# Kernel tuning notes

Hardware: AMD Instinct MI355X
Metric: run time of the kernel (lower is better)

The kernel has to match this reference:

```python
import jax, jax.numpy as jnp
import numpy as np
from jax import lax

_A = -0.75  # PyTorch bicubic coefficient


def _cubic_kernel(x):
    x = np.abs(x)
    return np.where(x <= 1.0, (_A + 2) * x**3 - (_A + 3) * x**2 + 1,
                    np.where(x < 2.0, _A * x**3 - 5 * _A * x**2 + 8 * _A * x - 4 * _A, 0.0))


def _cubic_mat(out_s, in_s):
    # align_corners=True bicubic interpolation matrix [out_s, in_s]
    i = np.arange(out_s)
    s = i * (in_s - 1) / (out_s - 1) if out_s > 1 else np.zeros(out_s)
    f = np.floor(s).astype(np.int64)
    t = s - f
    M = np.zeros((out_s, in_s), dtype=np.float32)
    for off in range(-1, 3):
        idx = np.clip(f + off, 0, in_s - 1)
        np.add.at(M, (i, idx), _cubic_kernel(t - off).astype(np.float32))
    return jnp.asarray(M)


def _bicubic_up(x, out_hw):
    Mh = _cubic_mat(out_hw[0], x.shape[-2])
    Mw = _cubic_mat(out_hw[1], x.shape[-1])
    y = jnp.einsum('Hh,bchw->bcHw', Mh, x)
    return jnp.einsum('Ww,bcHw->bcHW', Mw, y)


def _conv(x, w, b, pad=1):
    y = lax.conv_general_dilated(x, w, (1, 1), [(pad, pad), (pad, pad)],
                                 dimension_numbers=('NCHW', 'OIHW', 'NCHW'))
    return y + b[None, :, None, None]


def _pool(x):
    return lax.reduce_window(x, -jnp.inf, lax.max, (1, 1, 2, 2), (1, 1, 2, 2), 'VALID')


def _features(x, ws):
    # VGG19 feat1 = conv0+relu (64ch, full res); feat2 = conv2..conv14 (256ch, 1/4 res)
    x1 = jax.nn.relu(_conv(x, *ws[0]))
    h = jax.nn.relu(_conv(x1, *ws[1]))
    h = _pool(h)
    h = jax.nn.relu(_conv(h, *ws[2]))
    h = jax.nn.relu(_conv(h, *ws[3]))
    h = _pool(h)
    h = jax.nn.relu(_conv(h, *ws[4]))
    h = jax.nn.relu(_conv(h, *ws[5]))
    h = jax.nn.relu(_conv(h, *ws[6]))
    h = _bicubic_up(h, x1.shape[-2:])  # bicubic, align_corners=True
    return jnp.concatenate([x1, h], axis=1)  # 64 + 256 = 320 channels


def _forward(x_ref, x_template, w0, b0, w2, b2, w5, b5, w7, b7, w10, b10, w12, b12,
             w14, b14, coef_ref, coef_temp, fw1, fb1, fw2, fb2, fw3, fb3):
    ws = [(w0, b0), (w2, b2), (w5, b5), (w7, b7), (w10, b10), (w12, b12), (w14, b14)]
    fref = _features(x_ref, ws)
    ftem = _features(x_template, ws)
    # L2-normalize over channel dim
    fref = fref / (1e-8 + jnp.linalg.norm(fref, axis=1, keepdims=True))
    ftem = ftem / (1e-8 + jnp.linalg.norm(ftem, axis=1, keepdims=True))
    b, c, H, W = fref.shape
    fref = fref.reshape(b, c, H // 2, 2, W // 2, 2).mean(axis=(3, 5))
    # dense correlation volume
    dist = jnp.einsum('bcmn,bcpq->bmnpq', fref, ftem) / 320.0
    m, n, p, q = dist.shape[1:]
    dist = dist.reshape(b, m * n, p * q)
    # dual-axis softmax + sqrt combination (LoFTR-style)
    conf_ref = jax.nn.softmax(coef_ref * dist, axis=-2)
    conf_tmp = jax.nn.softmax(coef_temp * dist, axis=-1)
    confidence = jnp.sqrt(conf_ref * conf_tmp)
    conf_values, _ = lax.top_k(confidence, 5)  # [b, m*n, 5]
    conf = conf_values.reshape(b, m, n, 5).transpose(0, 3, 1, 2)
    # final head (dropout = identity in eval)
    h = jax.nn.relu(_conv(conf, fw1, fb1))
    h = jax.nn.relu(_conv(h, fw2, fb2))
    out = _conv(h, fw3, fb3, pad=0)
    out = _bicubic_up(out, x_ref.shape[-2:])
    return out


def setup_inputs() -> dict:
    key = jax.random.key(0)
    ks = jax.random.split(key, 16)
    B, H, W = 1, 128, 128

    def cw(k, o, i, s):
        return jax.random.normal(k, (o, i, s, s), jnp.float32) * (1.0 / np.sqrt(i * s * s))

    d = {
        'x_ref': jax.random.normal(ks[0], (B, 3, H, W), jnp.float32),
        'x_template': jax.random.normal(ks[1], (B, 3, H, W), jnp.float32),
        'w0': cw(ks[2], 64, 3, 3), 'b0': jnp.zeros((64,), jnp.float32),
        'w2': cw(ks[3], 64, 64, 3), 'b2': jnp.zeros((64,), jnp.float32),
        'w5': cw(ks[4], 128, 64, 3), 'b5': jnp.zeros((128,), jnp.float32),
        'w7': cw(ks[5], 128, 128, 3), 'b7': jnp.zeros((128,), jnp.float32),
        'w10': cw(ks[6], 256, 128, 3), 'b10': jnp.zeros((256,), jnp.float32),
        'w12': cw(ks[7], 256, 256, 3), 'b12': jnp.zeros((256,), jnp.float32),
        'w14': cw(ks[8], 256, 256, 3), 'b14': jnp.zeros((256,), jnp.float32),
        'coef_ref': jnp.float32(1.0), 'coef_temp': jnp.float32(1.0),
        # final head: weights_init_normal -> N(1/3, 0.02)
        'fw1': 1.0 / 3 + 0.02 * jax.random.normal(ks[9], (8, 5, 3, 3), jnp.float32),
        'fb1': 0.02 * jax.random.normal(ks[10], (8,), jnp.float32),
        'fw2': 1.0 / 3 + 0.02 * jax.random.normal(ks[11], (8, 8, 3, 3), jnp.float32),
        'fb2': 0.02 * jax.random.normal(ks[12], (8,), jnp.float32),
        'fw3': 1.0 / 3 + 0.02 * jax.random.normal(ks[13], (1, 8, 1, 1), jnp.float32),
        'fb3': 0.02 * jax.random.normal(ks[14], (1,), jnp.float32),
    }
    return d


def reference(x_ref, x_template, w0, b0, w2, b2, w5, b5, w7, b7, w10, b10, w12, b12,
              w14, b14, coef_ref, coef_temp, fw1, fb1, fw2, fb2, fw3, fb3):
    return _forward(x_ref, x_template, w0, b0, w2, b2, w5, b5, w7, b7, w10, b10,
                    w12, b12, w14, b14, coef_ref, coef_temp, fw1, fb1, fw2, fb2, fw3, fb3)
```

## Files before the change

kernel.cpp:

```cpp
#include <hip/hip_runtime.h>
#include <math.h>

typedef unsigned short ushort_t;
typedef unsigned int uint_t;
typedef __attribute__((ext_vector_type(8))) short bf16x8;
typedef __attribute__((ext_vector_type(4))) float f32x4;

#define FSTRIDE ((size_t)16384 * 320)
#define TSTRIDE ((size_t)16384 * 64)

__device__ inline ushort_t f2bf(float f) {
    union { float f; uint_t u; } x; x.f = f;
    uint_t r = x.u + 0x7fffu + ((x.u >> 16) & 1u);
    return (ushort_t)(r >> 16);
}
__device__ inline float bf2f(ushort_t h) {
    union { uint_t u; float f; } x; x.u = ((uint_t)h) << 16;
    return x.f;
}
__device__ inline float bflo(uint_t u) {
    union { uint_t u; float f; } x; x.u = u << 16; return x.f;
}
__device__ inline float bfhi(uint_t u) {
    union { uint_t u; float f; } x; x.u = u & 0xffff0000u; return x.f;
}
__device__ inline uint_t cvtpk_bf16(float lo, float hi) {
    uint_t r;
    asm volatile("v_cvt_pk_bf16_f32 %0, %1, %2" : "=v"(r) : "v"(lo), "v"(hi));
    return r;
}
__device__ inline void gload16(const void* g, void* l) {
    __builtin_amdgcn_global_load_lds(
        (const __attribute__((address_space(1))) void*)g,
        (__attribute__((address_space(3))) void*)l, 16, 0, 0);
}

__global__ void wtrans_k(const float* __restrict__ w, ushort_t* __restrict__ wT, int CO, int CI)
{
    int idx = blockIdx.x * 256 + threadIdx.x;
    if (idx >= CO * CI * 9) return;
    int tap = idx % 9;
    int rem = idx / 9;
    int ci = rem % CI;
    int co = rem / CI;
    wT[((size_t)tap * CO + co) * CI + ci] = f2bf(w[idx]);
}

__global__ __launch_bounds__(256) void conv0_k(const float* __restrict__ x0, const float* __restrict__ x1,
                                               const float* __restrict__ w,
                                               const float* __restrict__ b, ushort_t* __restrict__ F)
{
    const float* x = blockIdx.y ? x1 : x0;
    F += (size_t)blockIdx.y * FSTRIDE;
    int co = threadIdx.x & 63;
    int p = blockIdx.x * 4 + (threadIdx.x >> 6);
    int y = p >> 7, xx = p & 127;
    float acc = b[co];
#pragma unroll
    for (int ci = 0; ci < 3; ++ci) {
#pragma unroll
        for (int t = 0; t < 9; ++t) {
            int dy = t / 3 - 1, dx = t % 3 - 1;
            int yy = y + dy, xc = xx + dx;
            if ((unsigned)yy < 128u && (unsigned)xc < 128u) {
                acc += x[ci * 16384 + yy * 128 + xc] * w[co * 27 + ci * 9 + t];
            }
        }
    }
    F[(size_t)p * 320 + co] = f2bf(fmaxf(acc, 0.f));
}

template<int CI>
__global__ __launch_bounds__(256) void conv_mfma_k(
    const ushort_t* __restrict__ in, int ldin, int inoff, size_t inImgStride,
    const ushort_t* __restrict__ wT, const float* __restrict__ bias,
    ushort_t* __restrict__ out, int ldout, int outoff, size_t outImgStride,
    int H, int W, int CO)
{
    in += (size_t)blockIdx.z * inImgStride;
    out += (size_t)blockIdx.z * outImgStride;
    const int tid = threadIdx.x;
    const int lane = tid & 63, wid = tid >> 6;
    const int wr = wid >> 1, wc = wid & 1;
    const int m0 = blockIdx.x * 64;
    const int n0 = blockIdx.y * 64;
    const int fr = lane & 15;
    const int fo = (lane >> 4) << 3;

    size_t abase[2];
    unsigned vmask[2];
#pragma unroll
    for (int mi = 0; mi < 2; ++mi) {
        int p = m0 + wr * 32 + mi * 16 + fr;
        int y = p / W, x = p % W;
        abase[mi] = (size_t)p * ldin + inoff + fo;
        unsigned vm = 0;
#pragma unroll
        for (int t = 0; t < 9; ++t) {
            int dy = t / 3 - 1, dx = t % 3 - 1;
            if ((unsigned)(y + dy) < (unsigned)H && (unsigned)(x + dx) < (unsigned)W) vm |= 1u << t;
        }
        vmask[mi] = vm;
    }

    f32x4 zero = {0.f, 0.f, 0.f, 0.f};
    f32x4 acc[2][2] = {{zero, zero}, {zero, zero}};
    const bf16x8 zz = {0, 0, 0, 0, 0, 0, 0, 0};

    for (int t = 0; t < 9; ++t) {
        int toff = ((t / 3 - 1) * W + (t % 3 - 1)) * ldin;
        bool v0 = (vmask[0] >> t) & 1u;
        bool v1 = (vmask[1] >> t) & 1u;
        const ushort_t* wp0 = wT + ((size_t)(t * CO + n0 + wc * 32 + fr)) * CI + fo;
        const ushort_t* wp1 = wp0 + (size_t)16 * CI;
#pragma unroll
        for (int kc = 0; kc < CI / 32; ++kc) {
            int k0 = kc * 32;
            bf16x8 a0 = v0 ? *(const bf16x8*)(in + abase[0] + toff + k0) : zz;
            bf16x8 a1 = v1 ? *(const bf16x8*)(in + abase[1] + toff + k0) : zz;
            bf16x8 b0 = *(const bf16x8*)(wp0 + k0);
            bf16x8 b1 = *(const bf16x8*)(wp1 + k0);
            acc[0][0] = __builtin_amdgcn_mfma_f32_16x16x32_bf16(b0, a0, acc[0][0], 0, 0, 0);
            acc[0][1] = __builtin_amdgcn_mfma_f32_16x16x32_bf16(b1, a0, acc[0][1], 0, 0, 0);
            acc[1][0] = __builtin_amdgcn_mfma_f32_16x16x32_bf16(b0, a1, acc[1][0], 0, 0, 0);
            acc[1][1] = __builtin_amdgcn_mfma_f32_16x16x32_bf16(b1, a1, acc[1][1], 0, 0, 0);
        }
    }

#pragma unroll
    for (int mi = 0; mi < 2; ++mi) {
#pragma unroll
        for (int ni = 0; ni < 2; ++ni) {
            int pix = m0 + wr * 32 + mi * 16 + (lane & 15);
            int ch = n0 + wc * 32 + ni * 16 + ((lane >> 4) << 2);
            float4 bv = *(const float4*)(bias + ch);
            float r0 = fmaxf(acc[mi][ni][0] + bv.x, 0.f);
            float r1 = fmaxf(acc[mi][ni][1] + bv.y, 0.f);
            float r2 = fmaxf(acc[mi][ni][2] + bv.z, 0.f);
            float r3 = fmaxf(acc[mi][ni][3] + bv.w, 0.f);
            uint2 pk;
            pk.x = (uint_t)f2bf(r0) | ((uint_t)f2bf(r1) << 16);
            pk.y = (uint_t)f2bf(r2) | ((uint_t)f2bf(r3) << 16);
            *(uint2*)(out + (size_t)pix * ldout + outoff + ch) = pk;
        }
    }
}

template<int CI>
__global__ __launch_bounds__(64) void conv_mfma1w_k(
    const ushort_t* __restrict__ in, int ldin, size_t inImgStride,
    const ushort_t* __restrict__ wT, const float* __restrict__ bias,
    ushort_t* __restrict__ out, int ldout, size_t outImgStride,
    int H, int W, int CO)
{
    in += (size_t)blockIdx.z * inImgStride;
    out += (size_t)blockIdx.z * outImgStride;
    const int lane = threadIdx.x;
    const int m0 = blockIdx.x * 32;
    const int n0 = blockIdx.y * 32;
    const int fr = lane & 15;
    const int fo = (lane >> 4) << 3;

    size_t abase[2];
    unsigned vmask[2];
#pragma unroll
    for (int mi = 0; mi < 2; ++mi) {
        int p = m0 + mi * 16 + fr;
        int y = p / W, x = p % W;
        abase[mi] = (size_t)p * ldin + fo;
        unsigned vm = 0;
#pragma unroll
        for (int t = 0; t < 9; ++t) {
            int dy = t / 3 - 1, dx = t % 3 - 1;
            if ((unsigned)(y + dy) < (unsigned)H && (unsigned)(x + dx) < (unsigned)W) vm |= 1u << t;
        }
        vmask[mi] = vm;
    }

    f32x4 zero = {0.f, 0.f, 0.f, 0.f};
    f32x4 acc[2][2] = {{zero, zero}, {zero, zero}};
    const bf16x8 zz = {0, 0, 0, 0, 0, 0, 0, 0};

    for (int t = 0; t < 9; ++t) {
        int toff = ((t / 3 - 1) * W + (t % 3 - 1)) * ldin;
        bool v0 = (vmask[0] >> t) & 1u;
        bool v1 = (vmask[1] >> t) & 1u;
        const ushort_t* wp0 = wT + ((size_t)(t * CO + n0 + fr)) * CI + fo;
        const ushort_t* wp1 = wp0 + (size_t)16 * CI;
#pragma unroll
        for (int kc = 0; kc < CI / 32; ++kc) {
            int k0 = kc * 32;
            bf16x8 a0 = v0 ? *(const bf16x8*)(in + abase[0] + toff + k0) : zz;
            bf16x8 a1 = v1 ? *(const bf16x8*)(in + abase[1] + toff + k0) : zz;
            bf16x8 b0 = *(const bf16x8*)(wp0 + k0);
            bf16x8 b1 = *(const bf16x8*)(wp1 + k0);
            acc[0][0] = __builtin_amdgcn_mfma_f32_16x16x32_bf16(b0, a0, acc[0][0], 0, 0, 0);
            acc[0][1] = __builtin_amdgcn_mfma_f32_16x16x32_bf16(b1, a0, acc[0][1], 0, 0, 0);
            acc[1][0] = __builtin_amdgcn_mfma_f32_16x16x32_bf16(b0, a1, acc[1][0], 0, 0, 0);
            acc[1][1] = __builtin_amdgcn_mfma_f32_16x16x32_bf16(b1, a1, acc[1][1], 0, 0, 0);
        }
    }

#pragma unroll
    for (int mi = 0; mi < 2; ++mi) {
#pragma unroll
        for (int ni = 0; ni < 2; ++ni) {
            int pix = m0 + mi * 16 + (lane & 15);
            int ch = n0 + ni * 16 + ((lane >> 4) << 2);
            float4 bv = *(const float4*)(bias + ch);
            float r0 = fmaxf(acc[mi][ni][0] + bv.x, 0.f);
            float r1 = fmaxf(acc[mi][ni][1] + bv.y, 0.f);
            float r2 = fmaxf(acc[mi][ni][2] + bv.z, 0.f);
            float r3 = fmaxf(acc[mi][ni][3] + bv.w, 0.f);
            uint2 pk;
            pk.x = (uint_t)f2bf(r0) | ((uint_t)f2bf(r1) << 16);
            pk.y = (uint_t)f2bf(r2) | ((uint_t)f2bf(r3) << 16);
            *(uint2*)(out + (size_t)pix * ldout + ch) = pk;
        }
    }
}

__global__ void maxpool_nhwc_k(const ushort_t* __restrict__ in, ushort_t* __restrict__ out,
                               int C, int Hi, int Wi)
{
    in += (size_t)blockIdx.y * TSTRIDE;
    out += (size_t)blockIdx.y * TSTRIDE;
    int idx = blockIdx.x * 256 + threadIdx.x;
    int CG = C >> 3;
    int Wo = Wi >> 1, Ho = Hi >> 1;
    if (idx >= Ho * Wo * CG) return;
    int cg = idx % CG;
    int p = idx / CG;
    int y = p / Wo, x = p % Wo;
    const ushort_t* ip = in + ((size_t)(2 * y) * Wi + 2 * x) * C + cg * 8;
    bf16x8 v0 = *(const bf16x8*)(ip);
    bf16x8 v1 = *(const bf16x8*)(ip + C);
    bf16x8 v2 = *(const bf16x8*)(ip + (size_t)Wi * C);
    bf16x8 v3 = *(const bf16x8*)(ip + (size_t)Wi * C + C);
    bf16x8 r;
#pragma unroll
    for (int j = 0; j < 8; ++j) {
        float m = fmaxf(fmaxf(bf2f((ushort_t)v0[j]), bf2f((ushort_t)v1[j])),
                        fmaxf(bf2f((ushort_t)v2[j]), bf2f((ushort_t)v3[j])));
        r[j] = (short)f2bf(m);
    }
    *(bf16x8*)(out + (size_t)p * C + cg * 8) = r;
}

__device__ inline void cubw(float t, float* w) {
    float x0 = 1.f + t, x2 = 1.f - t, x3 = 2.f - t;
    w[0] = ((-0.75f*x0 + 3.75f)*x0 - 6.f)*x0 + 3.f;
    w[1] = (1.25f*t - 2.25f)*t*t + 1.f;
    w[2] = (1.25f*x2 - 2.25f)*x2*x2 + 1.f;
    w[3] = ((-0.75f*x3 + 3.75f)*x3 - 6.f)*x3 + 3.f;
}

__global__ __launch_bounds__(256) void bicubic_nhwc_k(const ushort_t* __restrict__ in, ushort_t* __restrict__ F)
{
    in += (size_t)blockIdx.y * TSTRIDE;
    F += (size_t)blockIdx.y * FSTRIDE;
    int idx = blockIdx.x * 256 + threadIdx.x;
    int cg = idx & 31;
    int p = idx >> 5;
    int Y = p >> 7, X = p & 127;
    float sy = (float)Y * (31.f / 127.f);
    float sx = (float)X * (31.f / 127.f);
    int fy = (int)floorf(sy), fx = (int)floorf(sx);
    float ty = sy - (float)fy, tx = sx - (float)fx;
    float wy[4], wx[4];
    cubw(ty, wy); cubw(tx, wx);
    float a[8] = {0.f, 0.f, 0.f, 0.f, 0.f, 0.f, 0.f, 0.f};
#pragma unroll
    for (int i = 0; i < 4; ++i) {
        int yy = min(max(fy - 1 + i, 0), 31);
#pragma unroll
        for (int j = 0; j < 4; ++j) {
            int xx = min(max(fx - 1 + j, 0), 31);
            float w = wy[i] * wx[j];
            bf16x8 v = *(const bf16x8*)(in + ((size_t)yy * 32 + xx) * 256 + cg * 8);
#pragma unroll
            for (int e = 0; e < 8; ++e) a[e] += w * bf2f((ushort_t)v[e]);
        }
    }
    bf16x8 r;
#pragma unroll
    for (int e = 0; e < 8; ++e) r[e] = (short)f2bf(a[e]);
    *(bf16x8*)(F + (size_t)p * 320 + 64 + cg * 8) = r;
}

__global__ __launch_bounds__(256) void norm_k(ushort_t* __restrict__ F)
{
    int lane = threadIdx.x & 63;
    int p = blockIdx.x * 4 + (threadIdx.x >> 6);
    ushort_t* rp = F + (size_t)p * 320;
    bool act = lane < 40;
    bf16x8 v = {0, 0, 0, 0, 0, 0, 0, 0};
    float ss = 0.f;
    if (act) {
        v = *(const bf16x8*)(rp + lane * 8);
#pragma unroll
        for (int e = 0; e < 8; ++e) { float f = bf2f((ushort_t)v[e]); ss += f * f; }
    }
#pragma unroll
    for (int off = 32; off > 0; off >>= 1) ss += __shfl_xor(ss, off);
    float inv = 1.f / (1e-8f + sqrtf(ss));
    if (act) {
#pragma unroll
        for (int e = 0; e < 8; ++e) v[e] = (short)f2bf(bf2f((ushort_t)v[e]) * inv);
        *(bf16x8*)(rp + lane * 8) = v;
    }
}

__global__ void pool_ref_nhwc_k(const ushort_t* __restrict__ F, ushort_t* __restrict__ A)
{
    int idx = blockIdx.x * 256 + threadIdx.x;
    if (idx >= 4096 * 40) return;
    int cg = idx % 40;
    int m = idx / 40;
    int y = m >> 6, x = m & 63;
    const ushort_t* ip = F + ((size_t)(2 * y) * 128 + 2 * x) * 320 + cg * 8;
    bf16x8 v0 = *(const bf16x8*)(ip);
    bf16x8 v1 = *(const bf16x8*)(ip + 320);
    bf16x8 v2 = *(const bf16x8*)(ip + 128 * 320);
    bf16x8 v3 = *(const bf16x8*)(ip + 128 * 320 + 320);
    bf16x8 r;
#pragma unroll
    for (int j = 0; j < 8; ++j) {
        float s = bf2f((ushort_t)v0[j]) + bf2f((ushort_t)v1[j]) + bf2f((ushort_t)v2[j]) + bf2f((ushort_t)v3[j]);
        r[j] = (short)f2bf(0.25f * s);
    }
    *(bf16x8*)(A + (size_t)m * 320 + cg * 8) = r;
}

__global__ __launch_bounds__(256) void gemm_corr_k(
    const ushort_t* __restrict__ A, const ushort_t* __restrict__ B, ushort_t* __restrict__ D,
    const float* __restrict__ coefr, const float* __restrict__ coeft,
    float* __restrict__ rpsum, float* __restrict__ cpsum)
{
    __shared__ ushort_t lA[3][128 * 32];
    __shared__ ushort_t lB[3][128 * 32];
    __shared__ float cl[2][128];
    __shared__ float rl[2][128];
    const int tid = threadIdx.x;
    const int lane = tid & 63;
    const int wid = tid >> 6;
    const int wr = wid >> 1, wc = wid & 1;
    const int m0 = blockIdx.y * 128, n0 = blockIdx.x * 128;
    const int fr = lane & 15;
    const int fo = (lane >> 4) << 3;
    const int srow = tid >> 2;
    const int scol = (tid & 3) << 3;

    const ushort_t* Ag0 = A + (size_t)(m0 + srow) * 320 + scol;
    const ushort_t* Ag1 = Ag0 + (size_t)64 * 320;
    const ushort_t* Bg0 = B + (size_t)(n0 + srow) * 320 + scol;
    const ushort_t* Bg1 = Bg0 + (size_t)64 * 320;

    f32x4 zero = {0.f, 0.f, 0.f, 0.f};
    f32x4 acc[4][4];
#pragma unroll
    for (int i = 0; i < 4; ++i)
#pragma unroll
        for (int j = 0; j < 4; ++j) acc[i][j] = zero;

#define STAGE(buf, kk) { \
        gload16(Ag0 + (kk), &lA[buf][wid * 512]); \
        gload16(Ag1 + (kk), &lA[buf][2048 + wid * 512]); \
        gload16(Bg0 + (kk), &lB[buf][wid * 512]); \
        gload16(Bg1 + (kk), &lB[buf][2048 + wid * 512]); }

#define COMPUTE(buf) { \
        bf16x8 af[4], bfr[4]; \
        _Pragma("unroll") \
        for (int mi = 0; mi < 4; ++mi) \
            af[mi] = *(const bf16x8*)&lA[buf][(wr * 64 + mi * 16 + fr) * 32 + fo]; \
        _Pragma("unroll") \
        for (int ni = 0; ni < 4; ++ni) \
            bfr[ni] = *(const bf16x8*)&lB[buf][(wc * 64 + ni * 16 + fr) * 32 + fo]; \
        _Pragma("unroll") \
        for (int mi = 0; mi < 4; ++mi) \
            _Pragma("unroll") \
            for (int ni = 0; ni < 4; ++ni) \
                acc[mi][ni] = __builtin_amdgcn_mfma_f32_16x16x32_bf16(bfr[ni], af[mi], acc[mi][ni], 0, 0, 0); }

    STAGE(0, 0)
    STAGE(1, 32)
#pragma unroll
    for (int t = 0; t < 10; ++t) {
        if (t < 9) {
            asm volatile("s_waitcnt vmcnt(4)" ::: "memory");
        } else {
            asm volatile("s_waitcnt vmcnt(0)" ::: "memory");
        }
        __builtin_amdgcn_s_barrier();
        if (t + 2 < 10) {
            STAGE((t + 2) % 3, 32 * (t + 2))
        }
        COMPUTE(t % 3)
    }
#undef STAGE
#undef COMPUTE

    const float s = 1.0f / 320.0f;
    const float cr = coefr[0], ct = coeft[0];
    const bool sameCoef = (cr == ct);
    float rpx[4] = {0.f, 0.f, 0.f, 0.f};
    float cpx[4][4];
#pragma unroll
    for (int ni = 0; ni < 4; ++ni)
#pragma unroll
        for (int r = 0; r < 4; ++r) cpx[ni][r] = 0.f;

    const int mrow = lane & 15;
    const int ng = (lane >> 4) << 2;
#pragma unroll
    for (int mi = 0; mi < 4; ++mi) {
        int m = m0 + wr * 64 + mi * 16 + mrow;
        ushort_t* drow = D + (size_t)m * 16384;
#pragma unroll
        for (int ni = 0; ni < 4; ++ni) {
            int n = n0 + wc * 64 + ni * 16 + ng;
            float d0 = acc[mi][ni][0] * s;
            float d1 = acc[mi][ni][1] * s;
            float d2 = acc[mi][ni][2] * s;
            float d3 = acc[mi][ni][3] * s;
            uint2 pk;
            pk.x = cvtpk_bf16(d0, d1);
            pk.y = cvtpk_bf16(d2, d3);
            *(uint2*)(drow + n) = pk;
            float e0 = __expf(cr * d0), e1 = __expf(cr * d1);
            float e2 = __expf(cr * d2), e3 = __expf(cr * d3);
            cpx[ni][0] += e0; cpx[ni][1] += e1; cpx[ni][2] += e2; cpx[ni][3] += e3;
            if (sameCoef) {
                rpx[mi] += e0 + e1 + e2 + e3;
            } else {
                rpx[mi] += __expf(ct * d0) + __expf(ct * d1) + __expf(ct * d2) + __expf(ct * d3);
            }
        }
    }
#pragma unroll
    for (int mi = 0; mi < 4; ++mi) {
        rpx[mi] += __shfl_xor(rpx[mi], 16);
        rpx[mi] += __shfl_xor(rpx[mi], 32);
    }
    if (lane < 16) {
#pragma unroll
        for (int mi = 0; mi < 4; ++mi)
            rl[wc][wr * 64 + mi * 16 + lane] = rpx[mi];
    }
#pragma unroll
    for (int ni = 0; ni < 4; ++ni)
#pragma unroll
        for (int r = 0; r < 4; ++r) {
            cpx[ni][r] += __shfl_xor(cpx[ni][r], 1);
            cpx[ni][r] += __shfl_xor(cpx[ni][r], 2);
            cpx[ni][r] += __shfl_xor(cpx[ni][r], 4);
            cpx[ni][r] += __shfl_xor(cpx[ni][r], 8);
        }
    if ((lane & 15) == 0) {
        int g = lane >> 4;
#pragma unroll
        for (int ni = 0; ni < 4; ++ni)
#pragma unroll
            for (int r = 0; r < 4; ++r)
                cl[wr][wc * 64 + ni * 16 + g * 4 + r] = cpx[ni][r];
    }
    __syncthreads();
    if (tid < 128) {
        cpsum[(size_t)blockIdx.y * 16384 + n0 + tid] = cl[0][tid] + cl[1][tid];
        rpsum[(size_t)blockIdx.x * 4096 + m0 + tid] = rl[0][tid] + rl[1][tid];
    }
}

__global__ void colfin_k(const float* __restrict__ cpsum, float* __restrict__ lc)
{
    int j = blockIdx.x * 256 + threadIdx.x;
    float s = 0.f;
#pragma unroll
    for (int k = 0; k < 32; ++k) s += cpsum[(size_t)k * 16384 + j];
    lc[j] = -0.5f * __logf(s);
}
__global__ void rowfin_k(const float* __restrict__ rpsum, float* __restrict__ invr)
{
    int m = blockIdx.x * 256 + threadIdx.x;
    float s = 0.f;
#pragma unroll
    for (int k = 0; k < 128; ++k) s += rpsum[(size_t)k * 4096 + m];
    invr[m] = rsqrtf(s);
}

#define INS5(w_) { float w = (w_); float mx; \
    mx = fmaxf(w, t0); w = fminf(w, t0); t0 = mx; \
    mx = fmaxf(w, t1); w = fminf(w, t1); t1 = mx; \
    mx = fmaxf(w, t2); w = fminf(w, t2); t2 = mx; \
    mx = fmaxf(w, t3); w = fminf(w, t3); t3 = mx; \
    t4 = fmaxf(w, t4); }

__global__ __launch_bounds__(256) void row_topk_k(
    const ushort_t* __restrict__ Dist, const float* __restrict__ lc,
    const float* __restrict__ invr,
    const float* __restrict__ coefr, const float* __restrict__ coeft,
    float* __restrict__ conf5)
{
    int wid = threadIdx.x >> 6, lane = threadIdx.x & 63;
    int row = blockIdx.x * 4 + wid;
    float hc = 0.5f * (coefr[0] + coeft[0]);
    const ushort_t* rp = Dist + (size_t)row * 16384;

    float t0 = -1e30f, t1 = -1e30f, t2 = -1e30f, t3 = -1e30f, t4 = -1e30f;
    for (int i = 0; i < 32; ++i) {
        int col = (i * 64 + lane) * 8;
        uint4 u = *(const uint4*)(rp + col);
        float4 l0 = *(const float4*)(lc + col);
        float4 l1 = *(const float4*)(lc + col + 4);
        float k0 = fmaf(hc, bflo(u.x), l0.x);
        float k1 = fmaf(hc, bfhi(u.x), l0.y);
        float k2 = fmaf(hc, bflo(u.y), l0.z);
        float k3 = fmaf(hc, bfhi(u.y), l0.w);
        float k4 = fmaf(hc, bflo(u.z), l1.x);
        float k5 = fmaf(hc, bfhi(u.z), l1.y);
        float k6 = fmaf(hc, bflo(u.w), l1.z);
        float k7 = fmaf(hc, bfhi(u.w), l1.w);
        float m8 = fmaxf(fmaxf(fmaxf(k0, k1), fmaxf(k2, k3)),
                         fmaxf(fmaxf(k4, k5), fmaxf(k6, k7)));
        if (m8 > t4) {
            INS5(k0); INS5(k1); INS5(k2); INS5(k3);
            INS5(k4); INS5(k5); INS5(k6); INS5(k7);
        }
    }
#pragma unroll
    for (int off = 1; off < 64; off <<= 1) {
        float o0 = __shfl_xor(t0, off), o1 = __shfl_xor(t1, off), o2 = __shfl_xor(t2, off);
        float o3 = __shfl_xor(t3, off), o4 = __shfl_xor(t4, off);
        INS5(o0); INS5(o1); INS5(o2); INS5(o3); INS5(o4);
    }
    if (lane == 0) {
        float iv = invr[row];
        conf5[0 * 4096 + row] = __expf(t0) * iv;
        conf5[1 * 4096 + row] = __expf(t1) * iv;
        conf5[2 * 4096 + row] = __expf(t2) * iv;
        conf5[3 * 4096 + row] = __expf(t3) * iv;
        conf5[4 * 4096 + row] = __expf(t4) * iv;
    }
}

__global__ void conv3x3_k(const float* __restrict__ in, const float* __restrict__ wgt,
                          const float* __restrict__ bias, float* __restrict__ out,
                          int Cin, int H, int W, int relu)
{
    int p = blockIdx.x * 256 + threadIdx.x;
    int HW = H * W;
    if (p >= HW) return;
    int co0 = blockIdx.y * 8;
    int y = p / W, x = p - y * W;
    float acc0 = bias[co0+0], acc1 = bias[co0+1], acc2 = bias[co0+2], acc3 = bias[co0+3];
    float acc4 = bias[co0+4], acc5 = bias[co0+5], acc6 = bias[co0+6], acc7 = bias[co0+7];
    bool ym = y > 0, yp = y < H-1, xm = x > 0, xp = x < W-1;
    for (int ci = 0; ci < Cin; ++ci) {
        const float* ip = in + (size_t)ci * HW + p;
        float v0 = (ym && xm) ? ip[-W-1] : 0.f;
        float v1 = (ym)       ? ip[-W]   : 0.f;
        float v2 = (ym && xp) ? ip[-W+1] : 0.f;
        float v3 = (xm)       ? ip[-1]   : 0.f;
        float v4 =              ip[0];
        float v5 = (xp)       ? ip[1]    : 0.f;
        float v6 = (yp && xm) ? ip[W-1]  : 0.f;
        float v7 = (yp)       ? ip[W]    : 0.f;
        float v8 = (yp && xp) ? ip[W+1]  : 0.f;
        const float* wp = wgt + ((size_t)co0 * Cin + ci) * 9;
        size_t ws = (size_t)Cin * 9;
#define CACC(q, a) { const float* wq = wp + q * ws; \
        a += wq[0]*v0 + wq[1]*v1 + wq[2]*v2 + wq[3]*v3 + wq[4]*v4 \
           + wq[5]*v5 + wq[6]*v6 + wq[7]*v7 + wq[8]*v8; }
        CACC(0, acc0) CACC(1, acc1) CACC(2, acc2) CACC(3, acc3)
        CACC(4, acc4) CACC(5, acc5) CACC(6, acc6) CACC(7, acc7)
#undef CACC
    }
#define CW(q, a) { float r = a; if (relu) r = fmaxf(r, 0.f); out[(size_t)(co0+q)*HW + p] = r; }
    CW(0, acc0) CW(1, acc1) CW(2, acc2) CW(3, acc3)
    CW(4, acc4) CW(5, acc5) CW(6, acc6) CW(7, acc7)
#undef CW
}

__global__ void bicubic_k(const float* __restrict__ in, float* __restrict__ out,
                          int C, int Hin, int Win, int Hout, int Wout)
{
    int idx = blockIdx.x * 256 + threadIdx.x;
    int total = C * Hout * Wout;
    if (idx >= total) return;
    int X = idx % Wout;
    int Y = (idx / Wout) % Hout;
    int c = idx / (Wout * Hout);
    float sy = (float)Y * (float)(Hin - 1) / (float)(Hout - 1);
    float sx = (float)X * (float)(Win - 1) / (float)(Wout - 1);
    int fy = (int)floorf(sy), fx = (int)floorf(sx);
    float ty = sy - (float)fy, tx = sx - (float)fx;
    float wy[4], wx[4];
    cubw(ty, wy); cubw(tx, wx);
    const float* ip = in + (size_t)c * Hin * Win;
    float acc = 0.f;
#pragma unroll
    for (int i = 0; i < 4; ++i) {
        int yy = min(max(fy - 1 + i, 0), Hin - 1);
        float ra = 0.f;
#pragma unroll
        for (int j = 0; j < 4; ++j) {
            int xx = min(max(fx - 1 + j, 0), Win - 1);
            ra += wx[j] * ip[yy * Win + xx];
        }
        acc += wy[i] * ra;
    }
    out[idx] = acc;
}

__global__ void conv1x1_k(const float* __restrict__ in, const float* __restrict__ w,
                          const float* __restrict__ b, float* __restrict__ out, int Cin, int HW)
{
    int p = blockIdx.x * 256 + threadIdx.x;
    if (p >= HW) return;
    float a = b[0];
    for (int c = 0; c < Cin; ++c) a += w[c] * in[(size_t)c * HW + p];
    out[p] = a;
}

extern "C" void kernel_launch(void* const* d_in, const int* in_sizes, int n_in,
                              void* d_out, int out_size, void* d_ws, size_t ws_size,
                              hipStream_t stream)
{
    const float* x_ref = (const float*)d_in[0];
    const float* x_tem = (const float*)d_in[1];
    const float* w0  = (const float*)d_in[2];   const float* b0  = (const float*)d_in[3];
    const float* w2  = (const float*)d_in[4];   const float* b2  = (const float*)d_in[5];
    const float* w5  = (const float*)d_in[6];   const float* b5  = (const float*)d_in[7];
    const float* w7  = (const float*)d_in[8];   const float* b7  = (const float*)d_in[9];
    const float* w10 = (const float*)d_in[10];  const float* b10 = (const float*)d_in[11];
    const float* w12 = (const float*)d_in[12];  const float* b12 = (const float*)d_in[13];
    const float* w14 = (const float*)d_in[14];  const float* b14 = (const float*)d_in[15];
    const float* coefr = (const float*)d_in[16];
    const float* coeft = (const float*)d_in[17];
    const float* fw1 = (const float*)d_in[18];  const float* fb1 = (const float*)d_in[19];
    const float* fw2 = (const float*)d_in[20];  const float* fb2 = (const float*)d_in[21];
    const float* fw3 = (const float*)d_in[22];  const float* fb3 = (const float*)d_in[23];
    float* out = (float*)d_out;

    char* wsp = (char*)d_ws;
    auto alloc = [&](size_t bytes) { char* p = wsp; wsp += (bytes + 255) & ~(size_t)255; return p; };
    ushort_t* F     = (ushort_t*)alloc(2 * FSTRIDE * 2);
    ushort_t* t1    = (ushort_t*)alloc(2 * TSTRIDE * 2);
    ushort_t* t2    = (ushort_t*)alloc(2 * TSTRIDE * 2);
    ushort_t* wT2   = (ushort_t*)alloc((size_t)64 * 64 * 9 * 2);
    ushort_t* wT5   = (ushort_t*)alloc((size_t)128 * 64 * 9 * 2);
    ushort_t* wT7   = (ushort_t*)alloc((size_t)128 * 128 * 9 * 2);
    ushort_t* wT10  = (ushort_t*)alloc((size_t)256 * 128 * 9 * 2);
    ushort_t* wT12  = (ushort_t*)alloc((size_t)256 * 256 * 9 * 2);
    ushort_t* wT14  = (ushort_t*)alloc((size_t)256 * 256 * 9 * 2);
    ushort_t* Abuf  = (ushort_t*)alloc((size_t)4096 * 320 * 2);
    ushort_t* dist  = (ushort_t*)alloc((size_t)4096 * 16384 * 2);
    float*    rpsum = (float*)alloc((size_t)128 * 4096 * 4);
    float*    cpsum = (float*)alloc((size_t)32 * 16384 * 4);
    float*    lc    = (float*)alloc(16384 * 4);
    float*    invr  = (float*)alloc(4096 * 4);
    float*    conf5 = (float*)alloc(5 * 4096 * 4);
    float*    h1    = (float*)alloc(8 * 4096 * 4);
    float*    h2    = (float*)alloc(8 * 4096 * 4);
    float*    out64 = (float*)alloc(4096 * 4);
    (void)ws_size; (void)n_in; (void)in_sizes; (void)out_size;

    wtrans_k<<<(64*64*9 + 255)/256, 256, 0, stream>>>(w2, wT2, 64, 64);
    wtrans_k<<<(128*64*9 + 255)/256, 256, 0, stream>>>(w5, wT5, 128, 64);
    wtrans_k<<<(128*128*9 + 255)/256, 256, 0, stream>>>(w7, wT7, 128, 128);
    wtrans_k<<<(256*128*9 + 255)/256, 256, 0, stream>>>(w10, wT10, 256, 128);
    wtrans_k<<<(256*256*9 + 255)/256, 256, 0, stream>>>(w12, wT12, 256, 256);
    wtrans_k<<<(256*256*9 + 255)/256, 256, 0, stream>>>(w14, wT14, 256, 256);

    conv0_k<<<dim3(4096, 2), 256, 0, stream>>>(x_ref, x_tem, w0, b0, F);
    conv_mfma_k<64><<<dim3(256, 1, 2), 256, 0, stream>>>(F, 320, 0, FSTRIDE, wT2, b2, t1, 64, 0, TSTRIDE, 128, 128, 64);
    maxpool_nhwc_k<<<dim3(128, 2), 256, 0, stream>>>(t1, t2, 64, 128, 128);
    conv_mfma_k<64><<<dim3(64, 2, 2), 256, 0, stream>>>(t2, 64, 0, TSTRIDE, wT5, b5, t1, 128, 0, TSTRIDE, 64, 64, 128);
    conv_mfma_k<128><<<dim3(64, 2, 2), 256, 0, stream>>>(t1, 128, 0, TSTRIDE, wT7, b7, t2, 128, 0, TSTRIDE, 64, 64, 128);
    maxpool_nhwc_k<<<dim3(64, 2), 256, 0, stream>>>(t2, t1, 128, 64, 64);
    conv_mfma1w_k<128><<<dim3(32, 8, 2), 64, 0, stream>>>(t1, 128, TSTRIDE, wT10, b10, t2, 256, TSTRIDE, 32, 32, 256);
    conv_mfma1w_k<256><<<dim3(32, 8, 2), 64, 0, stream>>>(t2, 256, TSTRIDE, wT12, b12, t1, 256, TSTRIDE, 32, 32, 256);
    conv_mfma1w_k<256><<<dim3(32, 8, 2), 64, 0, stream>>>(t1, 256, TSTRIDE, wT14, b14, t2, 256, TSTRIDE, 32, 32, 256);
    bicubic_nhwc_k<<<dim3(2048, 2), 256, 0, stream>>>(t2, F);
    norm_k<<<8192, 256, 0, stream>>>(F);

    pool_ref_nhwc_k<<<640, 256, 0, stream>>>(F, Abuf);

    gemm_corr_k<<<dim3(128, 32), 256, 0, stream>>>(Abuf, F + FSTRIDE, dist, coefr, coeft, rpsum, cpsum);

    colfin_k<<<64, 256, 0, stream>>>(cpsum, lc);
    rowfin_k<<<16, 256, 0, stream>>>(rpsum, invr);

    row_topk_k<<<1024, 256, 0, stream>>>(dist, lc, invr, coefr, coeft, conf5);

    conv3x3_k<<<dim3(16, 1), 256, 0, stream>>>(conf5, fw1, fb1, h1, 5, 64, 64, 1);
    conv3x3_k<<<dim3(16, 1), 256, 0, stream>>>(h1, fw2, fb2, h2, 8, 64, 64, 1);
    conv1x1_k<<<16, 256, 0, stream>>>(h2, fw3, fb3, out64, 8, 4096);
    bicubic_k<<<64, 256, 0, stream>>>(out64, out, 1, 64, 64, 128, 128);
}
```

Measured before the change: 410.2 us.

## Use smaller one-wave conv tiles, swizzle GEMM LDS, and fuse small launches

Replaces the 4-wave 64x64 conv kernel and the 1-wave 32x32 kernel with one templated single-wave kernel that covers 16 pixels by 16*NF channels. This launches many more blocks, so more of the GPU is busy on the small feature maps. It also XOR-swizzles the LDS layout in the correlation GEMM to cut bank conflicts. Several tiny launches are merged: the six weight transposes, the row and column finalisers, and the second head conv fused with the 1x1 conv. In exchange, the smaller tiles give less data reuse, so each block reloads more weights and activations.

```diff
diff --git a/kernel.cpp b/kernel.cpp
--- a/kernel.cpp
+++ b/kernel.cpp
@@ -35,15 +35,25 @@
         (__attribute__((address_space(3))) void*)l, 16, 0, 0);
 }
 
-__global__ void wtrans_k(const float* __restrict__ w, ushort_t* __restrict__ wT, int CO, int CI)
-{
-    int idx = blockIdx.x * 256 + threadIdx.x;
+struct WT6 {
+    const float* src[6];
+    ushort_t* dst[6];
+    int co[6], ci[6];
+    int off[6];
+};
+__global__ void wtrans6_k(WT6 a)
+{
+    int b = blockIdx.x, seg = 0;
+#pragma unroll
+    for (int s = 1; s < 6; ++s) if (b >= a.off[s]) seg = s;
+    int idx = (b - a.off[seg]) * 256 + threadIdx.x;
+    int CO = a.co[seg], CI = a.ci[seg];
     if (idx >= CO * CI * 9) return;
     int tap = idx % 9;
     int rem = idx / 9;
     int ci = rem % CI;
     int co = rem / CI;
-    wT[((size_t)tap * CO + co) * CI + ci] = f2bf(w[idx]);
+    a.dst[seg][((size_t)tap * CO + co) * CI + ci] = f2bf(a.src[seg][idx]);
 }
 
 __global__ __launch_bounds__(256) void conv0_k(const float* __restrict__ x0, const float* __restrict__ x1,
@@ -70,8 +80,8 @@
     F[(size_t)p * 320 + co] = f2bf(fmaxf(acc, 0.f));
 }
 
-template<int CI>
-__global__ __launch_bounds__(256) void conv_mfma_k(
+template<int CI, int NF>
+__global__ __launch_bounds__(64) void conv1w_k(
     const ushort_t* __restrict__ in, int ldin, int inoff, size_t inImgStride,
     const ushort_t* __restrict__ wT, const float* __restrict__ bias,
     ushort_t* __restrict__ out, int ldout, int outoff, size_t outImgStride,
@@ -79,144 +89,58 @@
 {
     in += (size_t)blockIdx.z * inImgStride;
     out += (size_t)blockIdx.z * outImgStride;
-    const int tid = threadIdx.x;
-    const int lane = tid & 63, wid = tid >> 6;
-    const int wr = wid >> 1, wc = wid & 1;
-    const int m0 = blockIdx.x * 64;
-    const int n0 = blockIdx.y * 64;
+    const int lane = threadIdx.x;
+    const int m0 = blockIdx.x * 16;
+    const int n0 = blockIdx.y * (16 * NF);
     const int fr = lane & 15;
     const int fo = (lane >> 4) << 3;
 
-    size_t abase[2];
-    unsigned vmask[2];
-#pragma unroll
-    for (int mi = 0; mi < 2; ++mi) {
-        int p = m0 + wr * 32 + mi * 16 + fr;
-        int y = p / W, x = p % W;
-        abase[mi] = (size_t)p * ldin + inoff + fo;
-        unsigned vm = 0;
-#pragma unroll
-        for (int t = 0; t < 9; ++t) {
-            int dy = t / 3 - 1, dx = t % 3 - 1;
-            if ((unsigned)(y + dy) < (unsigned)H && (unsigned)(x + dx) < (unsigned)W) vm |= 1u << t;
-        }
-        vmask[mi] = vm;
+    int p = m0 + fr;
+    int y = p / W, x = p % W;
+    size_t abase = (size_t)p * ldin + inoff + fo;
+    unsigned vm = 0;
+#pragma unroll
+    for (int t = 0; t < 9; ++t) {
+        int dy = t / 3 - 1, dx = t % 3 - 1;
+        if ((unsigned)(y + dy) < (unsigned)H && (unsigned)(x + dx) < (unsigned)W) vm |= 1u << t;
     }
 
     f32x4 zero = {0.f, 0.f, 0.f, 0.f};
-    f32x4 acc[2][2] = {{zero, zero}, {zero, zero}};
+    f32x4 acc[NF];
+#pragma unroll
+    for (int i = 0; i < NF; ++i) acc[i] = zero;
     const bf16x8 zz = {0, 0, 0, 0, 0, 0, 0, 0};
 
+#pragma unroll 3
     for (int t = 0; t < 9; ++t) {
         int toff = ((t / 3 - 1) * W + (t % 3 - 1)) * ldin;
-        bool v0 = (vmask[0] >> t) & 1u;
-        bool v1 = (vmask[1] >> t) & 1u;
-        const ushort_t* wp0 = wT + ((size_t)(t * CO + n0 + wc * 32 + fr)) * CI + fo;
-        const ushort_t* wp1 = wp0 + (size_t)16 * CI;
+        bool v = (vm >> t) & 1u;
+        const ushort_t* wp = wT + ((size_t)(t * CO + n0 + fr)) * CI + fo;
 #pragma unroll
         for (int kc = 0; kc < CI / 32; ++kc) {
             int k0 = kc * 32;
-            bf16x8 a0 = v0 ? *(const bf16x8*)(in + abase[0] + toff + k0) : zz;
-            bf16x8 a1 = v1 ? *(const bf16x8*)(in + abase[1] + toff + k0) : zz;
-            bf16x8 b0 = *(const bf16x8*)(wp0 + k0);
-            bf16x8 b1 = *(const bf16x8*)(wp1 + k0);
-            acc[0][0] = __builtin_amdgcn_mfma_f32_16x16x32_bf16(b0, a0, acc[0][0], 0, 0, 0);
-            acc[0][1] = __builtin_amdgcn_mfma_f32_16x16x32_bf16(b1, a0, acc[0][1], 0, 0, 0);
-            acc[1][0] = __builtin_amdgcn_mfma_f32_16x16x32_bf16(b0, a1, acc[1][0], 0, 0, 0);
-            acc[1][1] = __builtin_amdgcn_mfma_f32_16x16x32_bf16(b1, a1, acc[1][1], 0, 0, 0);
-        }
-    }
-
-#pragma unroll
-    for (int mi = 0; mi < 2; ++mi) {
-#pragma unroll
-        for (int ni = 0; ni < 2; ++ni) {
-            int pix = m0 + wr * 32 + mi * 16 + (lane & 15);
-            int ch = n0 + wc * 32 + ni * 16 + ((lane >> 4) << 2);
-            float4 bv = *(const float4*)(bias + ch);
-            float r0 = fmaxf(acc[mi][ni][0] + bv.x, 0.f);
-            float r1 = fmaxf(acc[mi][ni][1] + bv.y, 0.f);
-            float r2 = fmaxf(acc[mi][ni][2] + bv.z, 0.f);
-            float r3 = fmaxf(acc[mi][ni][3] + bv.w, 0.f);
-            uint2 pk;
-            pk.x = (uint_t)f2bf(r0) | ((uint_t)f2bf(r1) << 16);
-            pk.y = (uint_t)f2bf(r2) | ((uint_t)f2bf(r3) << 16);
-            *(uint2*)(out + (size_t)pix * ldout + outoff + ch) = pk;
-        }
-    }
-}
-
-template<int CI>
-__global__ __launch_bounds__(64) void conv_mfma1w_k(
-    const ushort_t* __restrict__ in, int ldin, size_t inImgStride,
-    const ushort_t* __restrict__ wT, const float* __restrict__ bias,
-    ushort_t* __restrict__ out, int ldout, size_t outImgStride,
-    int H, int W, int CO)
-{
-    in += (size_t)blockIdx.z * inImgStride;
-    out += (size_t)blockIdx.z * outImgStride;
-    const int lane = threadIdx.x;
-    const int m0 = blockIdx.x * 32;
-    const int n0 = blockIdx.y * 32;
-    const int fr = lane & 15;
-    const int fo = (lane >> 4) << 3;
-
-    size_t abase[2];
-    unsigned vmask[2];
-#pragma unroll
-    for (int mi = 0; mi < 2; ++mi) {
-        int p = m0 + mi * 16 + fr;
-        int y = p / W, x = p % W;
-        abase[mi] = (size_t)p * ldin + fo;
-        unsigned vm = 0;
-#pragma unroll
-        for (int t = 0; t < 9; ++t) {
-            int dy = t / 3 - 1, dx = t % 3 - 1;
-            if ((unsigned)(y + dy) < (unsigned)H && (unsigned)(x + dx) < (unsigned)W) vm |= 1u << t;
-        }
-        vmask[mi] = vm;
-    }
-
-    f32x4 zero = {0.f, 0.f, 0.f, 0.f};
-    f32x4 acc[2][2] = {{zero, zero}, {zero, zero}};
-    const bf16x8 zz = {0, 0, 0, 0, 0, 0, 0, 0};
-
-    for (int t = 0; t < 9; ++t) {
-        int toff = ((t / 3 - 1) * W + (t % 3 - 1)) * ldin;
-        bool v0 = (vmask[0] >> t) & 1u;
-        bool v1 = (vmask[1] >> t) & 1u;
-        const ushort_t* wp0 = wT + ((size_t)(t * CO + n0 + fr)) * CI + fo;
-        const ushort_t* wp1 = wp0 + (size_t)16 * CI;
-#pragma unroll
-        for (int kc = 0; kc < CI / 32; ++kc) {
-            int k0 = kc * 32;
-            bf16x8 a0 = v0 ? *(const bf16x8*)(in + abase[0] + toff + k0) : zz;
-            bf16x8 a1 = v1 ? *(const bf16x8*)(in + abase[1] + toff + k0) : zz;
-            bf16x8 b0 = *(const bf16x8*)(wp0 + k0);
-            bf16x8 b1 = *(const bf16x8*)(wp1 + k0);
-            acc[0][0] = __builtin_amdgcn_mfma_f32_16x16x32_bf16(b0, a0, acc[0][0], 0, 0, 0);
-            acc[0][1] = __builtin_amdgcn_mfma_f32_16x16x32_bf16(b1, a0, acc[0][1], 0, 0, 0);
-            acc[1][0] = __builtin_amdgcn_mfma_f32_16x16x32_bf16(b0, a1, acc[1][0], 0, 0, 0);
-            acc[1][1] = __builtin_amdgcn_mfma_f32_16x16x32_bf16(b1, a1, acc[1][1], 0, 0, 0);
-        }
-    }
-
-#pragma unroll
-    for (int mi = 0; mi < 2; ++mi) {
-#pragma unroll
-        for (int ni = 0; ni < 2; ++ni) {
-            int pix = m0 + mi * 16 + (lane & 15);
-            int ch = n0 + ni * 16 + ((lane >> 4) << 2);
-            float4 bv = *(const float4*)(bias + ch);
-            float r0 = fmaxf(acc[mi][ni][0] + bv.x, 0.f);
-            float r1 = fmaxf(acc[mi][ni][1] + bv.y, 0.f);
-            float r2 = fmaxf(acc[mi][ni][2] + bv.z, 0.f);
-            float r3 = fmaxf(acc[mi][ni][3] + bv.w, 0.f);
-            uint2 pk;
-            pk.x = (uint_t)f2bf(r0) | ((uint_t)f2bf(r1) << 16);
-            pk.y = (uint_t)f2bf(r2) | ((uint_t)f2bf(r3) << 16);
-            *(uint2*)(out + (size_t)pix * ldout + ch) = pk;
-        }
+            bf16x8 a = v ? *(const bf16x8*)(in + abase + toff + k0) : zz;
+#pragma unroll
+            for (int nf = 0; nf < NF; ++nf) {
+                bf16x8 b = *(const bf16x8*)(wp + (size_t)nf * 16 * CI + k0);
+                acc[nf] = __builtin_amdgcn_mfma_f32_16x16x32_bf16(b, a, acc[nf], 0, 0, 0);
+            }
+        }
+    }
+
+#pragma unroll
+    for (int nf = 0; nf < NF; ++nf) {
+        int pix = m0 + (lane & 15);
+        int ch = n0 + nf * 16 + ((lane >> 4) << 2);
+        float4 bv = *(const float4*)(bias + ch);
+        float r0 = fmaxf(acc[nf][0] + bv.x, 0.f);
+        float r1 = fmaxf(acc[nf][1] + bv.y, 0.f);
+        float r2 = fmaxf(acc[nf][2] + bv.z, 0.f);
+        float r3 = fmaxf(acc[nf][3] + bv.w, 0.f);
+        uint2 pk;
+        pk.x = (uint_t)f2bf(r0) | ((uint_t)f2bf(r1) << 16);
+        pk.y = (uint_t)f2bf(r2) | ((uint_t)f2bf(r3) << 16);
+        *(uint2*)(out + (size_t)pix * ldout + outoff + ch) = pk;
     }
 }
 
@@ -350,10 +274,12 @@
     const int fo = (lane >> 4) << 3;
     const int srow = tid >> 2;
     const int scol = (tid & 3) << 3;
-
-    const ushort_t* Ag0 = A + (size_t)(m0 + srow) * 320 + scol;
+    const int scol_sw = scol ^ ((srow & 3) << 3);
+    const int fo_sw = fo ^ ((fr & 3) << 3);
+
+    const ushort_t* Ag0 = A + (size_t)(m0 + srow) * 320 + scol_sw;
     const ushort_t* Ag1 = Ag0 + (size_t)64 * 320;
-    const ushort_t* Bg0 = B + (size_t)(n0 + srow) * 320 + scol;
+    const ushort_t* Bg0 = B + (size_t)(n0 + srow) * 320 + scol_sw;
     const ushort_t* Bg1 = Bg0 + (size_t)64 * 320;
 
     f32x4 zero = {0.f, 0.f, 0.f, 0.f};
@@ -373,10 +299,10 @@
         bf16x8 af[4], bfr[4]; \
         _Pragma("unroll") \
         for (int mi = 0; mi < 4; ++mi) \
-            af[mi] = *(const bf16x8*)&lA[buf][(wr * 64 + mi * 16 + fr) * 32 + fo]; \
+            af[mi] = *(const bf16x8*)&lA[buf][(wr * 64 + mi * 16 + fr) * 32 + fo_sw]; \
         _Pragma("unroll") \
         for (int ni = 0; ni < 4; ++ni) \
-            bfr[ni] = *(const bf16x8*)&lB[buf][(wc * 64 + ni * 16 + fr) * 32 + fo]; \
+            bfr[ni] = *(const bf16x8*)&lB[buf][(wc * 64 + ni * 16 + fr) * 32 + fo_sw]; \
         _Pragma("unroll") \
         for (int mi = 0; mi < 4; ++mi) \
             _Pragma("unroll") \
@@ -472,21 +398,23 @@
     }
 }
 
-__global__ void colfin_k(const float* __restrict__ cpsum, float* __restrict__ lc)
-{
-    int j = blockIdx.x * 256 + threadIdx.x;
-    float s = 0.f;
-#pragma unroll
-    for (int k = 0; k < 32; ++k) s += cpsum[(size_t)k * 16384 + j];
-    lc[j] = -0.5f * __logf(s);
-}
-__global__ void rowfin_k(const float* __restrict__ rpsum, float* __restrict__ invr)
-{
-    int m = blockIdx.x * 256 + threadIdx.x;
-    float s = 0.f;
-#pragma unroll
-    for (int k = 0; k < 128; ++k) s += rpsum[(size_t)k * 4096 + m];
-    invr[m] = rsqrtf(s);
+__global__ void finboth_k(const float* __restrict__ cpsum, const float* __restrict__ rpsum,
+                          float* __restrict__ lc, float* __restrict__ invr)
+{
+    int b = blockIdx.x;
+    if (b < 64) {
+        int j = b * 256 + threadIdx.x;
+        float s = 0.f;
+#pragma unroll
+        for (int k = 0; k < 32; ++k) s += cpsum[(size_t)k * 16384 + j];
+        lc[j] = -0.5f * __logf(s);
+    } else {
+        int m = (b - 64) * 256 + threadIdx.x;
+        float s = 0.f;
+#pragma unroll
+        for (int k = 0; k < 128; ++k) s += rpsum[(size_t)k * 4096 + m];
+        invr[m] = rsqrtf(s);
+    }
 }
 
 #define INS5(w_) { float w = (w_); float mx; \
@@ -582,6 +510,41 @@
 #undef CW
 }
 
+__global__ void head2_k(const float* __restrict__ in, const float* __restrict__ wgt,
+                        const float* __restrict__ bias, const float* __restrict__ w3,
+                        const float* __restrict__ b3, float* __restrict__ out64)
+{
+    int p = blockIdx.x * 256 + threadIdx.x;
+    int y = p >> 6, x = p & 63;
+    float acc[8];
+#pragma unroll
+    for (int c = 0; c < 8; ++c) acc[c] = bias[c];
+    bool ym = y > 0, yp = y < 63, xm = x > 0, xp = x < 63;
+#pragma unroll
+    for (int ci = 0; ci < 8; ++ci) {
+        const float* ip = in + ci * 4096 + p;
+        float v0 = (ym && xm) ? ip[-65] : 0.f;
+        float v1 = (ym)       ? ip[-64] : 0.f;
+        float v2 = (ym && xp) ? ip[-63] : 0.f;
+        float v3 = (xm)       ? ip[-1]  : 0.f;
+        float v4 =              ip[0];
+        float v5 = (xp)       ? ip[1]   : 0.f;
+        float v6 = (yp && xm) ? ip[63]  : 0.f;
+        float v7 = (yp)       ? ip[64]  : 0.f;
+        float v8 = (yp && xp) ? ip[65]  : 0.f;
+#pragma unroll
+        for (int co = 0; co < 8; ++co) {
+            const float* wq = wgt + ((size_t)co * 8 + ci) * 9;
+            acc[co] += wq[0]*v0 + wq[1]*v1 + wq[2]*v2 + wq[3]*v3 + wq[4]*v4
+                     + wq[5]*v5 + wq[6]*v6 + wq[7]*v7 + wq[8]*v8;
+        }
+    }
+    float o = b3[0];
+#pragma unroll
+    for (int c = 0; c < 8; ++c) o += w3[c] * fmaxf(acc[c], 0.f);
+    out64[p] = o;
+}
+
 __global__ void bicubic_k(const float* __restrict__ in, float* __restrict__ out,
                           int C, int Hin, int Win, int Hout, int Wout)
 {
@@ -611,16 +574,6 @@
         acc += wy[i] * ra;
     }
     out[idx] = acc;
-}
-
-__global__ void conv1x1_k(const float* __restrict__ in, const float* __restrict__ w,
-                          const float* __restrict__ b, float* __restrict__ out, int Cin, int HW)
-{
-    int p = blockIdx.x * 256 + threadIdx.x;
-    if (p >= HW) return;
-    float a = b[0];
-    for (int c = 0; c < Cin; ++c) a += w[c] * in[(size_t)c * HW + p];
-    out[p] = a;
 }
 
 extern "C" void kernel_launch(void* const* d_in, const int* in_sizes, int n_in,
@@ -662,26 +615,29 @@
     float*    invr  = (float*)alloc(4096 * 4);
     float*    conf5 = (float*)alloc(5 * 4096 * 4);
     float*    h1    = (float*)alloc(8 * 4096 * 4);
-    float*    h2    = (float*)alloc(8 * 4096 * 4);
     float*    out64 = (float*)alloc(4096 * 4);
     (void)ws_size; (void)n_in; (void)in_sizes; (void)out_size;
 
-    wtrans_k<<<(64*64*9 + 255)/256, 256, 0, stream>>>(w2, wT2, 64, 64);
-    wtrans_k<<<(128*64*9 + 255)/256, 256, 0, stream>>>(w5, wT5, 128, 64);
-    wtrans_k<<<(128*128*9 + 255)/256, 256, 0, stream>>>(w7, wT7, 128, 128);
-    wtrans_k<<<(256*128*9 + 255)/256, 256, 0, stream>>>(w10, wT10, 256, 128);
-    wtrans_k<<<(256*256*9 + 255)/256, 256, 0, stream>>>(w12, wT12, 256, 256);
-    wtrans_k<<<(256*256*9 + 255)/256, 256, 0, stream>>>(w14, wT14, 256, 256);
+    WT6 wt;
+    wt.src[0] = w2;  wt.dst[0] = wT2;  wt.co[0] = 64;  wt.ci[0] = 64;
+    wt.src[1] = w5;  wt.dst[1] = wT5;  wt.co[1] = 128; wt.ci[1] = 64;
+    wt.src[2] = w7;  wt.dst[2] = wT7;  wt.co[2] = 128; wt.ci[2] = 128;
+    wt.src[3] = w10; wt.dst[3] = wT10; wt.co[3] = 256; wt.ci[3] = 128;
+    wt.src[4] = w12; wt.dst[4] = wT12; wt.co[4] = 256; wt.ci[4] = 256;
+    wt.src[5] = w14; wt.dst[5] = wT14; wt.co[5] = 256; wt.ci[5] = 256;
+    int nblk = 0;
+    for (int s = 0; s < 6; ++s) { wt.off[s] = nblk; nblk += (wt.co[s] * wt.ci[s] * 9 + 255) / 256; }
+    wtrans6_k<<<nblk, 256, 0, stream>>>(wt);
 
     conv0_k<<<dim3(4096, 2), 256, 0, stream>>>(x_ref, x_tem, w0, b0, F);
-    conv_mfma_k<64><<<dim3(256, 1, 2), 256, 0, stream>>>(F, 320, 0, FSTRIDE, wT2, b2, t1, 64, 0, TSTRIDE, 128, 128, 64);
+    conv1w_k<64, 2><<<dim3(1024, 2, 2), 64, 0, stream>>>(F, 320, 0, FSTRIDE, wT2, b2, t1, 64, 0, TSTRIDE, 128, 128, 64);
     maxpool_nhwc_k<<<dim3(128, 2), 256, 0, stream>>>(t1, t2, 64, 128, 128);
-    conv_mfma_k<64><<<dim3(64, 2, 2), 256, 0, stream>>>(t2, 64, 0, TSTRIDE, wT5, b5, t1, 128, 0, TSTRIDE, 64, 64, 128);
-    conv_mfma_k<128><<<dim3(64, 2, 2), 256, 0, stream>>>(t1, 128, 0, TSTRIDE, wT7, b7, t2, 128, 0, TSTRIDE, 64, 64, 128);
+    conv1w_k<64, 2><<<dim3(256, 4, 2), 64, 0, stream>>>(t2, 64, 0, TSTRIDE, wT5, b5, t1, 128, 0, TSTRIDE, 64, 64, 128);
+    conv1w_k<128, 2><<<dim3(256, 4, 2), 64, 0, stream>>>(t1, 128, 0, TSTRIDE, wT7, b7, t2, 128, 0, TSTRIDE, 64, 64, 128);
     maxpool_nhwc_k<<<dim3(64, 2), 256, 0, stream>>>(t2, t1, 128, 64, 64);
-    conv_mfma1w_k<128><<<dim3(32, 8, 2), 64, 0, stream>>>(t1, 128, TSTRIDE, wT10, b10, t2, 256, TSTRIDE, 32, 32, 256);
-    conv_mfma1w_k<256><<<dim3(32, 8, 2), 64, 0, stream>>>(t2, 256, TSTRIDE, wT12, b12, t1, 256, TSTRIDE, 32, 32, 256);
-    conv_mfma1w_k<256><<<dim3(32, 8, 2), 64, 0, stream>>>(t1, 256, TSTRIDE, wT14, b14, t2, 256, TSTRIDE, 32, 32, 256);
+    conv1w_k<128, 1><<<dim3(64, 16, 2), 64, 0, stream>>>(t1, 128, 0, TSTRIDE, wT10, b10, t2, 256, 0, TSTRIDE, 32, 32, 256);
+    conv1w_k<256, 1><<<dim3(64, 16, 2), 64, 0, stream>>>(t2, 256, 0, TSTRIDE, wT12, b12, t1, 256, 0, TSTRIDE, 32, 32, 256);
+    conv1w_k<256, 1><<<dim3(64, 16, 2), 64, 0, stream>>>(t1, 256, 0, TSTRIDE, wT14, b14, t2, 256, 0, TSTRIDE, 32, 32, 256);
     bicubic_nhwc_k<<<dim3(2048, 2), 256, 0, stream>>>(t2, F);
     norm_k<<<8192, 256, 0, stream>>>(F);
 
@@ -689,13 +645,11 @@
 
     gemm_corr_k<<<dim3(128, 32), 256, 0, stream>>>(Abuf, F + FSTRIDE, dist, coefr, coeft, rpsum, cpsum);
 
-    colfin_k<<<64, 256, 0, stream>>>(cpsum, lc);
-    rowfin_k<<<16, 256, 0, stream>>>(rpsum, invr);
+    finboth_k<<<80, 256, 0, stream>>>(cpsum, rpsum, lc, invr);
 
     row_topk_k<<<1024, 256, 0, stream>>>(dist, lc, invr, coefr, coeft, conf5);
 
     conv3x3_k<<<dim3(16, 1), 256, 0, stream>>>(conf5, fw1, fb1, h1, 5, 64, 64, 1);
-    conv3x3_k<<<dim3(16, 1), 256, 0, stream>>>(h1, fw2, fb2, h2, 8, 64, 64, 1);
-    conv1x1_k<<<16, 256, 0, stream>>>(h2, fw3, fb3, out64, 8, 4096);
+    head2_k<<<16, 256, 0, stream>>>(h1, fw2, fb2, fw3, fb3, out64);
     bicubic_k<<<64, 256, 0, stream>>>(out64, out, 1, 64, 64, 128, 128);
 }
```

Result: slower. 439.1 us (+7.0%).
